# Optimization experiments

Hardware: AMD Instinct MI355X
Metric: run time of the kernel (lower is better)

## Reference

```python
import jax, jax.numpy as jnp
import numpy as np
from jax import lax

N, CIN, CINT, COUT, K, L, H, W = 8, 256, 192, 128, 3, 512, 128, 128
IMG = 3
EPS = 1e-8

def setup_inputs() -> dict:
    key = jax.random.key(0)
    ks = jax.random.split(key, 16)
    d = {}
    d["x"] = jax.random.normal(ks[0], (N, CIN, H, W), jnp.float32)
    d["v"] = jax.random.normal(ks[1], (N, L), jnp.float32)
    d["y"] = jax.random.normal(ks[2], (N, IMG, H, W), jnp.float32)
    d["noise1"] = jax.random.normal(ks[3], (N, 1, 2 * H, 2 * W), jnp.float32)
    d["noise2"] = jax.random.normal(ks[4], (N, 1, 2 * H, 2 * W), jnp.float32)
    # Up_Mod_Conv weight is stored transposed: [in, out, k, k]
    d["w_up"] = jax.random.normal(ks[5], (CIN, CINT, K, K), jnp.float32) * 0.05
    d["b_up"] = jnp.zeros((CINT,), jnp.float32)
    d["sw_up"] = jax.random.normal(ks[6], (CIN, L), jnp.float32)
    d["sb_up"] = jnp.zeros((CIN,), jnp.float32)
    d["w_conv"] = jax.random.normal(ks[7], (COUT, CINT, K, K), jnp.float32) * 0.05
    d["b_conv"] = jnp.zeros((COUT,), jnp.float32)
    d["sw_conv"] = jax.random.normal(ks[8], (CINT, L), jnp.float32)
    d["sb_conv"] = jnp.zeros((CINT,), jnp.float32)
    d["w_rgb"] = jax.random.normal(ks[9], (IMG, COUT, 1, 1), jnp.float32) * 0.05
    d["b_rgb"] = jnp.zeros((IMG,), jnp.float32)
    d["sw_rgb"] = jax.random.normal(ks[10], (COUT, L), jnp.float32)
    d["sb_rgb"] = jnp.zeros((COUT,), jnp.float32)
    d["ns1"] = jnp.float32(0.1)
    d["ns2"] = jnp.float32(0.1)
    return d

def _act(t):
    return jax.nn.leaky_relu(t, 0.2)

def _style(v, sw, sb):
    # s = Linear(v) + 1, per StyleGAN2 modulation
    return v @ sw.T + sb + 1.0

def _g_block(x, v, y, noise1, noise2, w_up, b_up, sw_up, sb_up,
             w_conv, b_conv, sw_conv, sb_conv, w_rgb, b_rgb, sw_rgb, sb_rgb, ns1, ns2):
    # --- upconv: modulated transposed conv (k=3, stride=2, pad=1, output_pad=1) ---
    # Algorithmic rewrite of the batch-as-groups trick: scale inputs by style,
    # convolve once with the shared weight, then demodulate the outputs.
    s = _style(v, sw_up, sb_up)                              # [N, CIN]
    xs = x * s[:, :, None, None]
    # conv_transpose2d(w:[in,out,k,k]) == conv with lhs_dilation and flipped kernel
    w_eq = jnp.flip(w_up, (2, 3)).transpose(1, 0, 2, 3)      # [CINT, CIN, k, k]
    h = lax.conv_general_dilated(xs, w_eq, window_strides=(1, 1),
                                 padding=((1, 2), (1, 2)), lhs_dilation=(2, 2),
                                 dimension_numbers=("NCHW", "OIHW", "NCHW"))  # [N,CINT,2H,2W]
    wsq = jnp.sum(w_up ** 2, (2, 3)).T                       # [CINT, CIN]
    sigma = jnp.sqrt(jnp.einsum("ni,oi->no", s ** 2, wsq) + EPS)
    h = h / sigma[:, :, None, None] + b_up[None, :, None, None]
    h = _act(h + ns1 * noise1)
    # --- conv: modulated 3x3 conv, pad=1 ---
    s = _style(v, sw_conv, sb_conv)                          # [N, CINT]
    hs = h * s[:, :, None, None]
    h2 = lax.conv_general_dilated(hs, w_conv, window_strides=(1, 1),
                                  padding=((1, 1), (1, 1)),
                                  dimension_numbers=("NCHW", "OIHW", "NCHW"))  # [N,COUT,2H,2W]
    wsq = jnp.sum(w_conv ** 2, (2, 3))                       # [COUT, CINT]
    sigma = jnp.sqrt(jnp.einsum("ni,oi->no", s ** 2, wsq) + EPS)
    h2 = h2 / sigma[:, :, None, None] + b_conv[None, :, None, None]
    h2 = _act(h2 + ns2 * noise2)
    # --- to_channels: modulated 1x1 conv, no demodulation ---
    s = _style(v, sw_rgb, sb_rgb)                            # [N, COUT]
    rgb = jnp.einsum("nihw,oi->nohw", h2 * s[:, :, None, None], w_rgb[:, :, 0, 0])
    rgb = rgb + b_rgb[None, :, None, None]
    # --- skip: bilinear upsample (align_corners=False == half-pixel) ---
    y_up = jax.image.resize(y, (y.shape[0], y.shape[1], 2 * y.shape[2], 2 * y.shape[3]),
                            method="bilinear")
    y_out = y_up + _act(rgb)
    return h2, y_out

def reference(x, v, y, noise1, noise2, w_up, b_up, sw_up, sb_up,
              w_conv, b_conv, sw_conv, sb_conv, w_rgb, b_rgb, sw_rgb, sb_rgb, ns1, ns2):
    return _g_block(x, v, y, noise1, noise2, w_up, b_up, sw_up, sb_up,
                    w_conv, b_conv, sw_conv, sb_conv, w_rgb, b_rgb, sw_rgb, sb_rgb, ns1, ns2)
```

## Files before the change

### kernel.cpp

```cpp
#include <hip/hip_runtime.h>


using bfrag = __attribute__((ext_vector_type(8))) short;
using ffrag = __attribute__((ext_vector_type(4))) float;

#define WS_S_UP      0
#define WS_ISIG_UP   2048
#define WS_S_CONV    3584
#define WS_ISIG_CONV 5120
#define WS_S_RGB     6144
#define WS_H_OFF     32768ull
#define H_ELEMS      (8ull*192*256*256)
#define WS_WUP_OFF   (WS_H_OFF + 2ull*H_ELEMS)
#define WUP_ELEMS    (9*8*12*64*8)
#define WS_WCONV_OFF (WS_WUP_OFF + 2ull*WUP_ELEMS)
#define WCONV_ELEMS  (9*6*8*64*8)

__device__ __forceinline__ unsigned short f2bf(float f) {
    unsigned u = __float_as_uint(f);
    return (unsigned short)((u + 0x7fffu + ((u >> 16) & 1u)) >> 16);
}

__global__ __launch_bounds__(256) void style_kernel(
    const float* __restrict__ v,
    const float* __restrict__ sw_up, const float* __restrict__ sb_up,
    const float* __restrict__ w_up,
    const float* __restrict__ sw_conv, const float* __restrict__ sb_conv,
    const float* __restrict__ w_conv,
    const float* __restrict__ sw_rgb, const float* __restrict__ sb_rgb,
    float* __restrict__ ws)
{
    const int n = blockIdx.x;
    const int t = threadIdx.x;
    __shared__ float sup[256];
    __shared__ float sconv[192];
    const float* vp = v + n * 512;
    {
        float a = 0.f;
        const float* r = sw_up + (size_t)t * 512;
        for (int l = 0; l < 512; ++l) a = fmaf(vp[l], r[l], a);
        float s = a + sb_up[t] + 1.0f;
        sup[t] = s;
        ws[WS_S_UP + n * 256 + t] = s;
    }
    if (t < 192) {
        float a = 0.f;
        const float* r = sw_conv + (size_t)t * 512;
        for (int l = 0; l < 512; ++l) a = fmaf(vp[l], r[l], a);
        float s = a + sb_conv[t] + 1.0f;
        sconv[t] = s;
        ws[WS_S_CONV + n * 192 + t] = s;
    }
    if (t < 128) {
        float a = 0.f;
        const float* r = sw_rgb + (size_t)t * 512;
        for (int l = 0; l < 512; ++l) a = fmaf(vp[l], r[l], a);
        ws[WS_S_RGB + n * 128 + t] = a + sb_rgb[t] + 1.0f;
    }
    __syncthreads();
    if (t < 192) {
        float sum = 0.f;
        for (int i = 0; i < 256; ++i) {
            const float* w = w_up + ((size_t)i * 192 + t) * 9;
            float wsq = 0.f;
            #pragma unroll
            for (int k = 0; k < 9; ++k) wsq = fmaf(w[k], w[k], wsq);
            sum = fmaf(sup[i] * sup[i], wsq, sum);
        }
        ws[WS_ISIG_UP + n * 192 + t] = 1.0f / sqrtf(sum + 1e-8f);
    }
    if (t < 128) {
        float sum = 0.f;
        for (int i = 0; i < 192; ++i) {
            const float* w = w_conv + ((size_t)t * 192 + i) * 9;
            float wsq = 0.f;
            #pragma unroll
            for (int k = 0; k < 9; ++k) wsq = fmaf(w[k], w[k], wsq);
            sum = fmaf(sconv[i] * sconv[i], wsq, sum);
        }
        ws[WS_ISIG_CONV + n * 128 + t] = 1.0f / sqrtf(sum + 1e-8f);
    }
}

__global__ __launch_bounds__(256) void prepack_up(
    const float* __restrict__ w_up, unsigned short* __restrict__ out)
{
    int t = blockIdx.x * 256 + threadIdx.x;
    if (t >= 9 * 8 * 12 * 64) return;
    int lane = t & 63;
    int f = t >> 6;
    int ob = f % 12;
    int rest = f / 12;
    int kc = rest & 7;
    int tap = rest >> 3;
    int o = ob * 16 + (lane & 15);
    int ci0 = kc * 32 + (lane >> 4) * 8;
    unsigned short tmp[8];
    #pragma unroll
    for (int e = 0; e < 8; ++e)
        tmp[e] = f2bf(w_up[((size_t)((ci0 + e) * 192 + o)) * 9 + tap]);
    *(int4*)&out[(size_t)t * 8] = *(const int4*)tmp;
}

__global__ __launch_bounds__(256) void prepack_conv(
    const float* __restrict__ w_conv, unsigned short* __restrict__ out)
{
    int t = blockIdx.x * 256 + threadIdx.x;
    if (t >= 9 * 6 * 8 * 64) return;
    int lane = t & 63;
    int f = t >> 6;
    int ob = f & 7;
    int rest = f >> 3;
    int kc = rest % 6;
    int tap = rest / 6;
    int o = ob * 16 + (lane & 15);
    int ci0 = kc * 32 + (lane >> 4) * 8;
    unsigned short tmp[8];
    #pragma unroll
    for (int e = 0; e < 8; ++e)
        tmp[e] = f2bf(w_conv[((size_t)(o * 192 + ci0 + e)) * 9 + tap]);
    *(int4*)&out[(size_t)t * 8] = *(const int4*)tmp;
}

__global__ __launch_bounds__(256) void prestyle_x(
    const float* __restrict__ x, const float* __restrict__ ws,
    unsigned short* __restrict__ xs)
{
    const int n = blockIdx.x >> 7;
    const int y = blockIdx.x & 127;
    const int tid = threadIdx.x;
    __shared__ unsigned short st[128 * 72];

    for (int cc0 = 0; cc0 < 256; cc0 += 64) {
        if (cc0) __syncthreads();
        for (int idx = tid; idx < 64 * 128; idx += 256) {
            int c = idx >> 7;
            int xx = idx & 127;
            float s = ws[WS_S_UP + n * 256 + cc0 + c];
            float val = x[(((size_t)n * 256 + cc0 + c) * 128 + y) * 128 + xx] * s;
            st[xx * 72 + c] = f2bf(val);
        }
        __syncthreads();
        for (int idx = tid; idx < 128 * 8; idx += 256) {
            int xp = idx >> 3;
            int part = idx & 7;
            int4 v = *(const int4*)&st[xp * 72 + part * 8];
            *(int4*)&xs[(((size_t)n * 128 + y) * 128 + xp) * 256 + cc0 + part * 8] = v;
        }
    }
}

__global__ __launch_bounds__(256, 4) void upconv_mfma(
    const unsigned short* __restrict__ xs, const unsigned short* __restrict__ wt,
    const float* __restrict__ b_up, const float* __restrict__ noise1,
    const float* __restrict__ ns1p, const float* __restrict__ ws,
    unsigned short* __restrict__ h)
{
    const int id  = blockIdx.x;
    const int w   = (id & 7) * 1024 + (id >> 3);
    const int n   = w >> 10;
    const int rem = w & 1023;
    const int oy  = rem >> 2;
    const int bx  = rem & 3;
    const int px  = bx & 1;
    const int O0  = (bx >> 1) * 96;
    const int py  = oy & 1;
    const int iy0 = oy >> 1;
    const int rows = 1 + py;
    const int ntx  = 1 + px;
    const int ntaps = rows * ntx;

    const int tid  = threadIdx.x;
    const int wave = __builtin_amdgcn_readfirstlane(tid >> 6);
    const int lane = tid & 63;
    const int lm = lane & 15, quad = lane >> 4, k0 = quad * 8;
    const int wy = wave >> 1;
    const int wx = wave & 1;

    __shared__ __align__(16) unsigned short As[2 * 132 * 40];

    const bfrag* Bf = (const bfrag*)wt;
    const int ob_base = (bx >> 1) * 6 + wx * 3;

    ffrag acc[4][3] = {};

    for (int kc = 0; kc < 8; ++kc) {
        const int c0 = kc * 32;
        __syncthreads();
        {
            const int tot = rows * 516;
            for (int idx = tid; idx < tot; idx += 256) {
                int r = idx / 516;
                int rem2 = idx - r * 516;
                int xx = rem2 >> 2, u = rem2 & 3;
                int iy = iy0 + r;
                int4 v = {0, 0, 0, 0};
                if (iy < 128 && xx < 128)
                    v = *(const int4*)&xs[(((size_t)n * 128 + iy) * 128 + xx) * 256 + c0 + u * 8];
                *(int4*)&As[(r * 132 + xx) * 40 + u * 8] = v;
            }
        }
        __syncthreads();
        for (int t = 0; t < ntaps; ++t) {
            int rs = (ntx == 2) ? (t >> 1) : t;
            int cs = (ntx == 2) ? (t & 1) : 0;
            int ky = py ? (rs ? 0 : 2) : 1;
            int kx = px ? (cs ? 0 : 2) : 1;
            const bfrag* bp = Bf + ((size_t)(((ky * 3 + kx) * 8 + kc) * 12 + ob_base)) * 64 + lane;
            bfrag b[3];
            #pragma unroll
            for (int tn = 0; tn < 3; ++tn)
                b[tn] = bp[tn * 64];
            #pragma unroll
            for (int tm = 0; tm < 4; ++tm) {
                bfrag a = *(const bfrag*)&As[(rs * 132 + wy * 64 + tm * 16 + lm + cs) * 40 + k0];
                #pragma unroll
                for (int tn = 0; tn < 3; ++tn)
                    acc[tm][tn] = __builtin_amdgcn_mfma_f32_16x16x32_bf16(a, b[tn], acc[tm][tn], 0, 0, 0);
            }
        }
    }

    const float ns1 = ns1p[0];
    const float* isig  = ws + WS_ISIG_UP + n * 192;
    const float* sconv = ws + WS_S_CONV + n * 192;
    #pragma unroll
    for (int tn = 0; tn < 3; ++tn) {
        const int o = O0 + wx * 48 + tn * 16 + lm;
        const float sg = isig[o];
        const float bb = b_up[o];
        const float sc = sconv[o];
        #pragma unroll
        for (int tm = 0; tm < 4; ++tm) {
            #pragma unroll
            for (int r = 0; r < 4; ++r) {
                int m = wy * 64 + tm * 16 + quad * 4 + r;
                int ox = 2 * m + px;
                float val = acc[tm][tn][r] * sg + bb
                          + ns1 * noise1[((size_t)n * 256 + oy) * 256 + ox];
                val = val > 0.f ? val : 0.2f * val;
                h[(((size_t)n * 256 + oy) * 256 + ox) * 192 + o] = f2bf(val * sc);
            }
        }
    }
}

__global__ __launch_bounds__(256, 4) void conv_mfma(
    const unsigned short* __restrict__ h, const unsigned short* __restrict__ wt,
    const float* __restrict__ b_conv, const float* __restrict__ noise2,
    const float* __restrict__ ns2p, const float* __restrict__ ws,
    float* __restrict__ h2)
{
    const int id  = blockIdx.x;
    const int w   = (id & 7) * 512 + (id >> 3);
    const int n   = w >> 9;
    const int rem = w & 511;
    const int oy  = rem >> 1;
    const int X0  = (rem & 1) * 128;
    const int tid  = threadIdx.x;
    const int wave = __builtin_amdgcn_readfirstlane(tid >> 6);
    const int lane = tid & 63;
    const int lm = lane & 15, quad = lane >> 4, k0 = quad * 8;
    const int wy = wave >> 1, wx = wave & 1;

    __shared__ __align__(16) unsigned short As[3 * 132 * 40];

    const bfrag* Bf = (const bfrag*)wt;
    const int ob_base = wx * 4;

    ffrag acc[4][4] = {};

    for (int kc = 0; kc < 6; ++kc) {
        const int c0 = kc * 32;
        __syncthreads();
        for (int idx = tid; idx < 1560; idx += 256) {
            int r = idx / 520;
            int rem2 = idx - r * 520;
            int xx = rem2 >> 2, u = rem2 & 3;
            int iy = oy - 1 + r;
            int ix = X0 - 1 + xx;
            int4 v = {0, 0, 0, 0};
            if (iy >= 0 && iy < 256 && ix >= 0 && ix < 256)
                v = *(const int4*)&h[(((size_t)n * 256 + iy) * 256 + ix) * 192 + c0 + u * 8];
            *(int4*)&As[(r * 132 + xx) * 40 + u * 8] = v;
        }
        __syncthreads();
        for (int dy = 0; dy < 3; ++dy) {
            for (int dx = 0; dx < 3; ++dx) {
                const bfrag* bp = Bf + ((size_t)(((dy * 3 + dx) * 6 + kc) * 8 + ob_base)) * 64 + lane;
                bfrag b[4];
                #pragma unroll
                for (int tn = 0; tn < 4; ++tn)
                    b[tn] = bp[tn * 64];
                #pragma unroll
                for (int tm = 0; tm < 4; ++tm) {
                    bfrag a = *(const bfrag*)&As[(dy * 132 + wy * 64 + tm * 16 + lm + dx) * 40 + k0];
                    #pragma unroll
                    for (int tn = 0; tn < 4; ++tn)
                        acc[tm][tn] = __builtin_amdgcn_mfma_f32_16x16x32_bf16(a, b[tn], acc[tm][tn], 0, 0, 0);
                }
            }
        }
    }

    const float ns2 = ns2p[0];
    const float* isig = ws + WS_ISIG_CONV + n * 128;
    #pragma unroll
    for (int tn = 0; tn < 4; ++tn) {
        const int o = wx * 64 + tn * 16 + lm;
        const float sg = isig[o];
        const float bb = b_conv[o];
        #pragma unroll
        for (int tm = 0; tm < 4; ++tm) {
            const int ox0 = X0 + wy * 64 + tm * 16 + quad * 4;
            float4 nz = *(const float4*)&noise2[((size_t)n * 256 + oy) * 256 + ox0];
            float4 outv;
            float val;
            val = acc[tm][tn][0] * sg + bb + ns2 * nz.x; outv.x = val > 0.f ? val : 0.2f * val;
            val = acc[tm][tn][1] * sg + bb + ns2 * nz.y; outv.y = val > 0.f ? val : 0.2f * val;
            val = acc[tm][tn][2] * sg + bb + ns2 * nz.z; outv.z = val > 0.f ? val : 0.2f * val;
            val = acc[tm][tn][3] * sg + bb + ns2 * nz.w; outv.w = val > 0.f ? val : 0.2f * val;
            *(float4*)&h2[(((size_t)n * 128 + o) * 256 + oy) * 256 + ox0] = outv;
        }
    }
}

__global__ __launch_bounds__(256) void rgb_kernel(
    const float* __restrict__ h2, const float* __restrict__ w_rgb,
    const float* __restrict__ b_rgb, const float* __restrict__ y,
    const float* __restrict__ ws, float* __restrict__ yout)
{
    const int bid = blockIdx.x;
    const int n   = bid >> 8;
    const int pix = ((bid & 255) << 8) + threadIdx.x;
    const int oy  = pix >> 8, ox = pix & 255;

    __shared__ float cw0[128], cw1[128], cw2[128];
    if (threadIdx.x < 128) {
        float s = ws[WS_S_RGB + n * 128 + threadIdx.x];
        cw0[threadIdx.x] = w_rgb[0 * 128 + threadIdx.x] * s;
        cw1[threadIdx.x] = w_rgb[1 * 128 + threadIdx.x] * s;
        cw2[threadIdx.x] = w_rgb[2 * 128 + threadIdx.x] * s;
    }
    __syncthreads();

    const float* hp = h2 + (size_t)n * 128 * 65536 + oy * 256 + ox;
    float a0 = 0.f, a1 = 0.f, a2 = 0.f;
    for (int i = 0; i < 128; ++i) {
        float hv = hp[(size_t)i * 65536];
        a0 = fmaf(hv, cw0[i], a0);
        a1 = fmaf(hv, cw1[i], a1);
        a2 = fmaf(hv, cw2[i], a2);
    }

    const int m = oy >> 1;
    int iy0, iy1; float wy0, wy1;
    if ((oy & 1) == 0) { iy0 = m > 0 ? m - 1 : 0; iy1 = m; wy0 = 0.25f; wy1 = 0.75f; }
    else               { iy0 = m; iy1 = m < 127 ? m + 1 : 127; wy0 = 0.75f; wy1 = 0.25f; }
    const int mm = ox >> 1;
    int ix0, ix1; float wx0, wx1;
    if ((ox & 1) == 0) { ix0 = mm > 0 ? mm - 1 : 0; ix1 = mm; wx0 = 0.25f; wx1 = 0.75f; }
    else               { ix0 = mm; ix1 = mm < 127 ? mm + 1 : 127; wx0 = 0.75f; wx1 = 0.25f; }

    float r[3] = { a0 + b_rgb[0], a1 + b_rgb[1], a2 + b_rgb[2] };
    #pragma unroll
    for (int c = 0; c < 3; ++c) {
        float t = r[c];
        t = t > 0.f ? t : 0.2f * t;
        const float* yp = y + ((size_t)n * 3 + c) * 128 * 128;
        float yu = wy0 * (wx0 * yp[iy0 * 128 + ix0] + wx1 * yp[iy0 * 128 + ix1])
                 + wy1 * (wx0 * yp[iy1 * 128 + ix0] + wx1 * yp[iy1 * 128 + ix1]);
        yout[(((size_t)n * 3 + c) * 256 + oy) * 256 + ox] = yu + t;
    }
}

extern "C" void kernel_launch(void* const* d_in, const int* in_sizes, int n_in,
                              void* d_out, int out_size, void* d_ws, size_t ws_size,
                              hipStream_t stream)
{
    const float* x       = (const float*)d_in[0];
    const float* v       = (const float*)d_in[1];
    const float* y       = (const float*)d_in[2];
    const float* noise1  = (const float*)d_in[3];
    const float* noise2  = (const float*)d_in[4];
    const float* w_up    = (const float*)d_in[5];
    const float* b_up    = (const float*)d_in[6];
    const float* sw_up   = (const float*)d_in[7];
    const float* sb_up   = (const float*)d_in[8];
    const float* w_conv  = (const float*)d_in[9];
    const float* b_conv  = (const float*)d_in[10];
    const float* sw_conv = (const float*)d_in[11];
    const float* sb_conv = (const float*)d_in[12];
    const float* w_rgb   = (const float*)d_in[13];
    const float* b_rgb   = (const float*)d_in[14];
    const float* sw_rgb  = (const float*)d_in[15];
    const float* sb_rgb  = (const float*)d_in[16];
    const float* ns1     = (const float*)d_in[17];
    const float* ns2     = (const float*)d_in[18];

    float* ws = (float*)d_ws;
    unsigned short* h       = (unsigned short*)((char*)d_ws + WS_H_OFF);
    unsigned short* wt_up   = (unsigned short*)((char*)d_ws + WS_WUP_OFF);
    unsigned short* wt_conv = (unsigned short*)((char*)d_ws + WS_WCONV_OFF);
    float* h2   = (float*)d_out;
    float* yout = h2 + (size_t)67108864;
    unsigned short* xs = (unsigned short*)d_out;

    style_kernel<<<8, 256, 0, stream>>>(v, sw_up, sb_up, w_up, sw_conv, sb_conv,
                                        w_conv, sw_rgb, sb_rgb, ws);
    prepack_up<<<216, 256, 0, stream>>>(w_up, wt_up);
    prepack_conv<<<108, 256, 0, stream>>>(w_conv, wt_conv);
    prestyle_x<<<1024, 256, 0, stream>>>(x, ws, xs);
    upconv_mfma<<<8192, 256, 0, stream>>>(xs, wt_up, b_up, noise1, ns1, ws, h);
    conv_mfma<<<4096, 256, 0, stream>>>(h, wt_conv, b_conv, noise2, ns2, ws, h2);
    rgb_kernel<<<2048, 256, 0, stream>>>(h2, w_rgb, b_rgb, y, ws, yout);
}
```

Measured before the change: 1.095 ms.

## Compute two output rows per block in upconv and conv to reuse weights

Both MFMA conv kernels now compute two output rows per workgroup, so each block stages one extra input row in LDS and every weight fragment loaded feeds twice as many MFMAs. In upconv, the two rows with the same parity share taps and weight loads. In conv, weight fragments for the next tap are double-buffered. Grid sizes are halved and launch bounds relaxed to 2 blocks per SM. The cost is more registers, with accumulators doubled, and lower occupancy.

```diff
diff --git a/kernel.cpp b/kernel.cpp
--- a/kernel.cpp
+++ b/kernel.cpp
@@ -150,25 +150,22 @@
     }
 }
 
-__global__ __launch_bounds__(256, 4) void upconv_mfma(
+__global__ __launch_bounds__(256, 2) void upconv_mfma(
     const unsigned short* __restrict__ xs, const unsigned short* __restrict__ wt,
     const float* __restrict__ b_up, const float* __restrict__ noise1,
     const float* __restrict__ ns1p, const float* __restrict__ ws,
     unsigned short* __restrict__ h)
 {
     const int id  = blockIdx.x;
-    const int w   = (id & 7) * 1024 + (id >> 3);
-    const int n   = w >> 10;
-    const int rem = w & 1023;
-    const int oy  = rem >> 2;
-    const int bx  = rem & 3;
-    const int px  = bx & 1;
-    const int O0  = (bx >> 1) * 96;
-    const int py  = oy & 1;
-    const int iy0 = oy >> 1;
-    const int rows = 1 + py;
-    const int ntx  = 1 + px;
-    const int ntaps = rows * ntx;
+    const int w   = (id & 7) * 512 + (id >> 3);
+    const int n   = w >> 9;
+    const int rem = w & 511;
+    const int j   = rem >> 3;
+    const int q   = (rem >> 2) & 1;
+    const int px  = (rem >> 1) & 1;
+    const int O0  = (rem & 1) * 96;
+    const int nrows = 2 + q;
+    const int ng    = (1 + q) * (1 + px);
 
     const int tid  = threadIdx.x;
     const int wave = __builtin_amdgcn_readfirstlane(tid >> 6);
@@ -177,23 +174,23 @@
     const int wy = wave >> 1;
     const int wx = wave & 1;
 
-    __shared__ __align__(16) unsigned short As[2 * 132 * 40];
+    __shared__ __align__(16) unsigned short As[3 * 132 * 40];
 
     const bfrag* Bf = (const bfrag*)wt;
-    const int ob_base = (bx >> 1) * 6 + wx * 3;
-
-    ffrag acc[4][3] = {};
+    const int ob_base = (rem & 1) * 6 + wx * 3;
+
+    ffrag acc[2][4][3] = {};
 
     for (int kc = 0; kc < 8; ++kc) {
         const int c0 = kc * 32;
         __syncthreads();
         {
-            const int tot = rows * 516;
+            const int tot = nrows * 516;
             for (int idx = tid; idx < tot; idx += 256) {
                 int r = idx / 516;
                 int rem2 = idx - r * 516;
                 int xx = rem2 >> 2, u = rem2 & 3;
-                int iy = iy0 + r;
+                int iy = 2 * j + r;
                 int4 v = {0, 0, 0, 0};
                 if (iy < 128 && xx < 128)
                     v = *(const int4*)&xs[(((size_t)n * 128 + iy) * 128 + xx) * 256 + c0 + u * 8];
@@ -201,22 +198,36 @@
             }
         }
         __syncthreads();
-        for (int t = 0; t < ntaps; ++t) {
-            int rs = (ntx == 2) ? (t >> 1) : t;
-            int cs = (ntx == 2) ? (t & 1) : 0;
-            int ky = py ? (rs ? 0 : 2) : 1;
-            int kx = px ? (cs ? 0 : 2) : 1;
-            const bfrag* bp = Bf + ((size_t)(((ky * 3 + kx) * 8 + kc) * 12 + ob_base)) * 64 + lane;
-            bfrag b[3];
-            #pragma unroll
-            for (int tn = 0; tn < 3; ++tn)
-                b[tn] = bp[tn * 64];
-            #pragma unroll
-            for (int tm = 0; tm < 4; ++tm) {
-                bfrag a = *(const bfrag*)&As[(rs * 132 + wy * 64 + tm * 16 + lm + cs) * 40 + k0];
+        bfrag ball[4][3];
+        #pragma unroll
+        for (int g = 0; g < 4; ++g) {
+            if (g < ng) {
+                int rs = px ? (g >> 1) : g;
+                int cs = px ? (g & 1) : 0;
+                int ky = q ? (rs ? 0 : 2) : 1;
+                int kx = px ? (cs ? 0 : 2) : 1;
+                const bfrag* p = Bf + ((size_t)(((ky * 3 + kx) * 8 + kc) * 12 + ob_base)) * 64 + lane;
                 #pragma unroll
-                for (int tn = 0; tn < 3; ++tn)
-                    acc[tm][tn] = __builtin_amdgcn_mfma_f32_16x16x32_bf16(a, b[tn], acc[tm][tn], 0, 0, 0);
+                for (int tn = 0; tn < 3; ++tn) ball[g][tn] = p[tn * 64];
+            }
+        }
+        #pragma unroll
+        for (int g = 0; g < 4; ++g) {
+            if (g < ng) {
+                int rs = px ? (g >> 1) : g;
+                int cs = px ? (g & 1) : 0;
+                #pragma unroll
+                for (int r01 = 0; r01 < 2; ++r01) {
+                    int arow = q ? (r01 + rs) : r01;
+                    #pragma unroll
+                    for (int tm = 0; tm < 4; ++tm) {
+                        bfrag a = *(const bfrag*)&As[(arow * 132 + wy * 64 + tm * 16 + lm + cs) * 40 + k0];
+                        #pragma unroll
+                        for (int tn = 0; tn < 3; ++tn)
+                            acc[r01][tm][tn] = __builtin_amdgcn_mfma_f32_16x16x32_bf16(
+                                a, ball[g][tn], acc[r01][tm][tn], 0, 0, 0);
+                    }
+                }
             }
         }
     }
@@ -225,37 +236,41 @@
     const float* isig  = ws + WS_ISIG_UP + n * 192;
     const float* sconv = ws + WS_S_CONV + n * 192;
     #pragma unroll
-    for (int tn = 0; tn < 3; ++tn) {
-        const int o = O0 + wx * 48 + tn * 16 + lm;
-        const float sg = isig[o];
-        const float bb = b_up[o];
-        const float sc = sconv[o];
+    for (int r01 = 0; r01 < 2; ++r01) {
+        const int oy = 4 * j + q + 2 * r01;
         #pragma unroll
-        for (int tm = 0; tm < 4; ++tm) {
-            #pragma unroll
-            for (int r = 0; r < 4; ++r) {
-                int m = wy * 64 + tm * 16 + quad * 4 + r;
-                int ox = 2 * m + px;
-                float val = acc[tm][tn][r] * sg + bb
-                          + ns1 * noise1[((size_t)n * 256 + oy) * 256 + ox];
-                val = val > 0.f ? val : 0.2f * val;
-                h[(((size_t)n * 256 + oy) * 256 + ox) * 192 + o] = f2bf(val * sc);
-            }
-        }
-    }
-}
-
-__global__ __launch_bounds__(256, 4) void conv_mfma(
+        for (int tn = 0; tn < 3; ++tn) {
+            const int o = O0 + wx * 48 + tn * 16 + lm;
+            const float sg = isig[o];
+            const float bb = b_up[o];
+            const float sc = sconv[o];
+            #pragma unroll
+            for (int tm = 0; tm < 4; ++tm) {
+                #pragma unroll
+                for (int r = 0; r < 4; ++r) {
+                    int m = wy * 64 + tm * 16 + quad * 4 + r;
+                    int ox = 2 * m + px;
+                    float val = acc[r01][tm][tn][r] * sg + bb
+                              + ns1 * noise1[((size_t)n * 256 + oy) * 256 + ox];
+                    val = val > 0.f ? val : 0.2f * val;
+                    h[(((size_t)n * 256 + oy) * 256 + ox) * 192 + o] = f2bf(val * sc);
+                }
+            }
+        }
+    }
+}
+
+__global__ __launch_bounds__(256, 2) void conv_mfma(
     const unsigned short* __restrict__ h, const unsigned short* __restrict__ wt,
     const float* __restrict__ b_conv, const float* __restrict__ noise2,
     const float* __restrict__ ns2p, const float* __restrict__ ws,
     float* __restrict__ h2)
 {
     const int id  = blockIdx.x;
-    const int w   = (id & 7) * 512 + (id >> 3);
-    const int n   = w >> 9;
-    const int rem = w & 511;
-    const int oy  = rem >> 1;
+    const int w   = (id & 7) * 256 + (id >> 3);
+    const int n   = w >> 8;
+    const int rem = w & 255;
+    const int oy0 = (rem >> 1) * 2;
     const int X0  = (rem & 1) * 128;
     const int tid  = threadIdx.x;
     const int wave = __builtin_amdgcn_readfirstlane(tid >> 6);
@@ -263,21 +278,21 @@
     const int lm = lane & 15, quad = lane >> 4, k0 = quad * 8;
     const int wy = wave >> 1, wx = wave & 1;
 
-    __shared__ __align__(16) unsigned short As[3 * 132 * 40];
+    __shared__ __align__(16) unsigned short As[4 * 132 * 40];
 
     const bfrag* Bf = (const bfrag*)wt;
     const int ob_base = wx * 4;
 
-    ffrag acc[4][4] = {};
+    ffrag acc[2][4][4] = {};
 
     for (int kc = 0; kc < 6; ++kc) {
         const int c0 = kc * 32;
         __syncthreads();
-        for (int idx = tid; idx < 1560; idx += 256) {
+        for (int idx = tid; idx < 2080; idx += 256) {
             int r = idx / 520;
             int rem2 = idx - r * 520;
             int xx = rem2 >> 2, u = rem2 & 3;
-            int iy = oy - 1 + r;
+            int iy = oy0 - 1 + r;
             int ix = X0 - 1 + xx;
             int4 v = {0, 0, 0, 0};
             if (iy >= 0 && iy < 256 && ix >= 0 && ix < 256)
@@ -285,19 +300,31 @@
             *(int4*)&As[(r * 132 + xx) * 40 + u * 8] = v;
         }
         __syncthreads();
-        for (int dy = 0; dy < 3; ++dy) {
-            for (int dx = 0; dx < 3; ++dx) {
-                const bfrag* bp = Bf + ((size_t)(((dy * 3 + dx) * 6 + kc) * 8 + ob_base)) * 64 + lane;
-                bfrag b[4];
+
+        bfrag bb[2][4];
+        {
+            const bfrag* p = Bf + ((size_t)((0 * 6 + kc) * 8 + ob_base)) * 64 + lane;
+            #pragma unroll
+            for (int tn = 0; tn < 4; ++tn) bb[0][tn] = p[tn * 64];
+        }
+        #pragma unroll
+        for (int t = 0; t < 9; ++t) {
+            const int cur = t & 1, nxt = cur ^ 1;
+            if (t < 8) {
+                const bfrag* p = Bf + ((size_t)(((t + 1) * 6 + kc) * 8 + ob_base)) * 64 + lane;
                 #pragma unroll
-                for (int tn = 0; tn < 4; ++tn)
-                    b[tn] = bp[tn * 64];
+                for (int tn = 0; tn < 4; ++tn) bb[nxt][tn] = p[tn * 64];
+            }
+            const int dy = t / 3, dx = t % 3;
+            #pragma unroll
+            for (int r01 = 0; r01 < 2; ++r01) {
                 #pragma unroll
                 for (int tm = 0; tm < 4; ++tm) {
-                    bfrag a = *(const bfrag*)&As[(dy * 132 + wy * 64 + tm * 16 + lm + dx) * 40 + k0];
+                    bfrag a = *(const bfrag*)&As[((r01 + dy) * 132 + wy * 64 + tm * 16 + lm + dx) * 40 + k0];
                     #pragma unroll
                     for (int tn = 0; tn < 4; ++tn)
-                        acc[tm][tn] = __builtin_amdgcn_mfma_f32_16x16x32_bf16(a, b[tn], acc[tm][tn], 0, 0, 0);
+                        acc[r01][tm][tn] = __builtin_amdgcn_mfma_f32_16x16x32_bf16(
+                            a, bb[cur][tn], acc[r01][tm][tn], 0, 0, 0);
                 }
             }
         }
@@ -306,21 +333,25 @@
     const float ns2 = ns2p[0];
     const float* isig = ws + WS_ISIG_CONV + n * 128;
     #pragma unroll
-    for (int tn = 0; tn < 4; ++tn) {
-        const int o = wx * 64 + tn * 16 + lm;
-        const float sg = isig[o];
-        const float bb = b_conv[o];
+    for (int r01 = 0; r01 < 2; ++r01) {
+        const int oy = oy0 + r01;
         #pragma unroll
-        for (int tm = 0; tm < 4; ++tm) {
-            const int ox0 = X0 + wy * 64 + tm * 16 + quad * 4;
-            float4 nz = *(const float4*)&noise2[((size_t)n * 256 + oy) * 256 + ox0];
-            float4 outv;
-            float val;
-            val = acc[tm][tn][0] * sg + bb + ns2 * nz.x; outv.x = val > 0.f ? val : 0.2f * val;
-            val = acc[tm][tn][1] * sg + bb + ns2 * nz.y; outv.y = val > 0.f ? val : 0.2f * val;
-            val = acc[tm][tn][2] * sg + bb + ns2 * nz.z; outv.z = val > 0.f ? val : 0.2f * val;
-            val = acc[tm][tn][3] * sg + bb + ns2 * nz.w; outv.w = val > 0.f ? val : 0.2f * val;
-            *(float4*)&h2[(((size_t)n * 128 + o) * 256 + oy) * 256 + ox0] = outv;
+        for (int tn = 0; tn < 4; ++tn) {
+            const int o = wx * 64 + tn * 16 + lm;
+            const float sg = isig[o];
+            const float bb2 = b_conv[o];
+            #pragma unroll
+            for (int tm = 0; tm < 4; ++tm) {
+                const int ox0 = X0 + wy * 64 + tm * 16 + quad * 4;
+                float4 nz = *(const float4*)&noise2[((size_t)n * 256 + oy) * 256 + ox0];
+                float4 outv;
+                float val;
+                val = acc[r01][tm][tn][0] * sg + bb2 + ns2 * nz.x; outv.x = val > 0.f ? val : 0.2f * val;
+                val = acc[r01][tm][tn][1] * sg + bb2 + ns2 * nz.y; outv.y = val > 0.f ? val : 0.2f * val;
+                val = acc[r01][tm][tn][2] * sg + bb2 + ns2 * nz.z; outv.z = val > 0.f ? val : 0.2f * val;
+                val = acc[r01][tm][tn][3] * sg + bb2 + ns2 * nz.w; outv.w = val > 0.f ? val : 0.2f * val;
+                *(float4*)&h2[(((size_t)n * 128 + o) * 256 + oy) * 256 + ox0] = outv;
+            }
         }
     }
 }
@@ -411,7 +442,7 @@
     prepack_up<<<216, 256, 0, stream>>>(w_up, wt_up);
     prepack_conv<<<108, 256, 0, stream>>>(w_conv, wt_conv);
     prestyle_x<<<1024, 256, 0, stream>>>(x, ws, xs);
-    upconv_mfma<<<8192, 256, 0, stream>>>(xs, wt_up, b_up, noise1, ns1, ws, h);
-    conv_mfma<<<4096, 256, 0, stream>>>(h, wt_conv, b_conv, noise2, ns2, ws, h2);
+    upconv_mfma<<<4096, 256, 0, stream>>>(xs, wt_up, b_up, noise1, ns1, ws, h);
+    conv_mfma<<<2048, 256, 0, stream>>>(h, wt_conv, b_conv, noise2, ns2, ws, h2);
     rgb_kernel<<<2048, 256, 0, stream>>>(h2, w_rgb, b_rgb, y, ws, yout);
 }
```

After: 1.027 ms. 1.07x faster.
